# Performance work log

Hardware: AMD Instinct MI355X
Metric: run time of the kernel (lower is better)

Reference implementation:

```python
import jax, jax.numpy as jnp
import numpy as np

D_MODEL = 1024
NUM_HEADS = 16
HEAD_DIM = D_MODEL // NUM_HEADS


def setup_inputs() -> dict:
    key = jax.random.key(0)
    k_x, k_wqkv, k_bqkv, k_wo, k_bo = jax.random.split(key, 5)
    bound_qkv = 1.0 / np.sqrt(D_MODEL)
    x = jax.random.normal(k_x, (2, 2048, D_MODEL), dtype=jnp.float32)
    # torch nn.Linear init: U(-1/sqrt(fan_in), 1/sqrt(fan_in))
    W_qkv = jax.random.uniform(k_wqkv, (D_MODEL, 3 * D_MODEL), jnp.float32, -bound_qkv, bound_qkv)
    b_qkv = jax.random.uniform(k_bqkv, (3 * D_MODEL,), jnp.float32, -bound_qkv, bound_qkv)
    W_out = jax.random.uniform(k_wo, (D_MODEL, D_MODEL), jnp.float32, -bound_qkv, bound_qkv)
    b_out = jax.random.uniform(k_bo, (D_MODEL,), jnp.float32, -bound_qkv, bound_qkv)
    return {"x": x, "W_qkv": W_qkv, "b_qkv": b_qkv, "W_out": W_out, "b_out": b_out}


def reference(x, W_qkv, b_qkv, W_out, b_out):
    B, T, C = x.shape
    H, Dh = NUM_HEADS, HEAD_DIM
    qkv = x @ W_qkv + b_qkv                      # [B,T,3C]
    q, k, v = jnp.split(qkv, 3, axis=-1)
    # [B,T,C] -> [B,H,T,Dh]
    def to_heads(t):
        return t.reshape(B, T, H, Dh).transpose(0, 2, 1, 3)
    q, k, v = to_heads(q), to_heads(k), to_heads(v)
    scale = 1.0 / np.sqrt(Dh).astype(np.float32)
    scores = jnp.einsum("bhqd,bhkd->bhqk", q, k) * scale   # [B,H,T,T]
    weights = jax.nn.softmax(scores, axis=-1)
    attn = jnp.einsum("bhqk,bhkd->bhqd", weights, v)        # [B,H,T,Dh]
    attn = attn.transpose(0, 2, 1, 3).reshape(B, T, C)
    return attn @ W_out + b_out
```

## Files before the change

### kernel.cpp

```cpp
#include <hip/hip_runtime.h>

typedef __bf16 bf16x8 __attribute__((ext_vector_type(8)));
typedef float f32x4 __attribute__((ext_vector_type(4)));
typedef float f32x16 __attribute__((ext_vector_type(16)));

#define MFMA16(a, b, c) __builtin_amdgcn_mfma_f32_16x16x32_bf16(a, b, c, 0, 0, 0)
#define MFMA32(a, b, c) __builtin_amdgcn_mfma_f32_32x32x16_bf16(a, b, c, 0, 0, 0)
#define GLDS16(g, l)                                                              \
  __builtin_amdgcn_global_load_lds((const __attribute__((address_space(1))) void*)(g), \
                                   (__attribute__((address_space(3))) void*)(l), 16, 0, 0)

static __device__ __forceinline__ unsigned cvt_pk_bf16(float lo, float hi) {
  unsigned r;
  asm("v_cvt_pk_bf16_f32 %0, %1, %2" : "=v"(r) : "v"(lo), "v"(hi));
  return r;
}
static __device__ __forceinline__ void permswap(unsigned& a, unsigned& b) {
  asm("v_permlane32_swap_b32 %0, %1" : "+v"(a), "+v"(b));
}

__global__ __launch_bounds__(256) void cvt_bf16_kernel(const float* __restrict__ in,
                                                       __bf16* __restrict__ out, int n4) {
  int i = blockIdx.x * 256 + threadIdx.x;
  if (i < n4) {
    float4 v = ((const float4*)in)[i];
    union { __bf16 b[4]; uint2 u; } t;
    t.b[0] = (__bf16)v.x; t.b[1] = (__bf16)v.y;
    t.b[2] = (__bf16)v.z; t.b[3] = (__bf16)v.w;
    ((uint2*)out)[i] = t.u;
  }
}

__global__ __launch_bounds__(256) void transpose_w_kernel(const float* __restrict__ Wq,
                                                          __bf16* __restrict__ WqT,
                                                          const float* __restrict__ Wo,
                                                          __bf16* __restrict__ WoT) {
  const int Kd = 1024;
  int bx = blockIdx.x;
  const float* W; __bf16* WT; int Nd, n0;
  if (bx < 96) { W = Wq; WT = WqT; Nd = 3072; n0 = bx * 32; }
  else         { W = Wo; WT = WoT; Nd = 1024; n0 = (bx - 96) * 32; }
  __shared__ float tile[32][33];
  int k0 = blockIdx.y * 32;
  int tid = threadIdx.x;
  int kk = tid >> 3, nn = (tid & 7) * 4;
  float4 v = *(const float4*)&W[(size_t)(k0 + kk) * Nd + n0 + nn];
  tile[kk][nn] = v.x; tile[kk][nn + 1] = v.y;
  tile[kk][nn + 2] = v.z; tile[kk][nn + 3] = v.w;
  __syncthreads();
  int n2 = tid >> 3, k2 = (tid & 7) * 4;
  union { __bf16 b[4]; uint2 u; } t;
  t.b[0] = (__bf16)tile[k2][n2];
  t.b[1] = (__bf16)tile[k2 + 1][n2];
  t.b[2] = (__bf16)tile[k2 + 2][n2];
  t.b[3] = (__bf16)tile[k2 + 3][n2];
  *(uint2*)&WT[(size_t)(n0 + n2) * Kd + k0 + k2] = t.u;
}

template <bool OUT_F32, int NT>
__global__ __launch_bounds__(256) void gemm_kernel(const __bf16* __restrict__ A,
                                                   const __bf16* __restrict__ BT,
                                                   const float* __restrict__ bias,
                                                   void* __restrict__ Cout, int N,
                                                   int qn, float qs) {
  const int K = 1024;
  const int NJ = NT / 32;
  __shared__ __align__(16) __bf16 As[128 * 32];
  __shared__ __align__(16) __bf16 Bs[NT * 32];
  int tid = threadIdx.x;
  int wave = tid >> 6, lane = tid & 63;
  int quad = lane >> 4, l16 = lane & 15;
  int m0 = blockIdx.x * 128, n0 = blockIdx.y * NT;
  int wm = (wave >> 1) * 64, wn = (wave & 1) * (NT / 2);

  int srow = tid >> 2, scol = (tid & 3) * 8;
  const __bf16* aptr = A + (size_t)(m0 + srow) * K + scol;
  const __bf16* bptr = BT + (size_t)(n0 + srow) * K + scol;
  __bf16* asl = &As[(size_t)wave * 512];
  __bf16* bsl = &Bs[(size_t)wave * 512];

  f32x4 acc[4][NJ] = {};
  for (int k0 = 0; k0 < K; k0 += 32) {
    GLDS16(aptr + k0, asl);
    GLDS16(aptr + (size_t)64 * K + k0, asl + 2048);
    GLDS16(bptr + k0, bsl);
    if (NT == 128) GLDS16(bptr + (size_t)64 * K + k0, bsl + 2048);
    __syncthreads();
    bf16x8 af[4], bf[NJ];
    for (int i = 0; i < 4; i++)
      af[i] = *(bf16x8*)&As[(wm + i * 16 + l16) * 32 + quad * 8];
    for (int j = 0; j < NJ; j++)
      bf[j] = *(bf16x8*)&Bs[(wn + j * 16 + l16) * 32 + quad * 8];
    for (int i = 0; i < 4; i++)
      for (int j = 0; j < NJ; j++)
        acc[i][j] = MFMA16(af[i], bf[j], acc[i][j]);
    __syncthreads();
  }
  for (int j = 0; j < NJ; j++) {
    int col = n0 + wn + j * 16 + l16;
    float bv = bias[col];
    float sc = (col < qn) ? qs : 1.0f;
    for (int i = 0; i < 4; i++) {
      int rowb = m0 + wm + i * 16 + quad * 4;
      for (int r = 0; r < 4; r++) {
        float v = (acc[i][j][r] + bv) * sc;
        if (OUT_F32)
          ((float*)Cout)[(size_t)(rowb + r) * N + col] = v;
        else
          ((__bf16*)Cout)[(size_t)(rowb + r) * N + col] = (__bf16)v;
      }
    }
  }
}

__global__ __launch_bounds__(256) void transpose_v_kernel(const __bf16* __restrict__ qkv,
                                                          __bf16* __restrict__ Vt) {
  const int T = 2048, C3 = 3072;
  __shared__ __align__(16) __bf16 tile[64][72];
  int t0 = blockIdx.x * 64;
  int h = blockIdx.y, b = blockIdx.z;
  int tid = threadIdx.x;
  int tt = tid >> 2, c = (tid & 3) * 16;
  const __bf16* src = qkv + (size_t)(b * T + t0 + tt) * C3 + 2048 + h * 64 + c;
  *(uint4*)&tile[tt][c] = *(const uint4*)src;
  *(uint4*)&tile[tt][c + 8] = *(const uint4*)(src + 8);
  __syncthreads();
  int dd = tid >> 2, t2 = (tid & 3) * 16;
  union { __bf16 b_[16]; uint4 u[2]; } o;
  for (int i = 0; i < 16; i++) o.b_[i] = tile[t2 + i][dd];
  __bf16* dst = Vt + ((size_t)(b * 16 + h) * 64 + dd) * T + t0 + t2;
  *(uint4*)dst = o.u[0];
  *(uint4*)(dst + 8) = o.u[1];
}

__global__ __launch_bounds__(256, 2) void attn_kernel(const __bf16* __restrict__ qkv,
                                                      const __bf16* __restrict__ Vt,
                                                      __bf16* __restrict__ O) {
  const int T = 2048, C3 = 3072;
  int p = blockIdx.x * 4 + (blockIdx.y >> 4);
  int b = p >> 4, h = p & 15;
  int q0 = (blockIdx.y & 15) * 128;

  int tid = threadIdx.x, wave = tid >> 6, lane = tid & 63;
  int l32 = lane & 31, hi = lane >> 5;

  __shared__ __align__(16) __bf16 Ks[2][64 * 64];
  __shared__ __align__(16) __bf16 Vs[2][64 * 64];

  const __bf16* qp = qkv + (size_t)(b * T + q0 + wave * 32 + l32) * C3 + h * 64;
  bf16x8 qf[4];
#pragma unroll
  for (int ds = 0; ds < 4; ds++)
    qf[ds] = *(const bf16x8*)(qp + ds * 16 + hi * 8);

  const __bf16* kbase = qkv + (size_t)(b * T) * C3 + 1024 + h * 64;
  const __bf16* vbase = Vt + (size_t)(b * 16 + h) * 64 * T;

  int srow = wave * 8 + (lane >> 3);
  int scol = ((lane & 7) ^ (lane >> 3)) * 8;
  const __bf16* ksrc = kbase + (size_t)srow * C3 + scol;
  const __bf16* vsrc = vbase + (size_t)srow * T + scol;

  int off[2][4];
#pragma unroll
  for (int rb = 0; rb < 2; rb++)
#pragma unroll
    for (int c4 = 0; c4 < 4; c4++)
      off[rb][c4] = (rb * 32 + l32) * 64 + (((c4 * 2 + hi) ^ (l32 & 7)) * 8);

  f32x16 o[2] = {};
  float rs = 0.0f;

  GLDS16(ksrc, &Ks[0][wave * 512]);
  GLDS16(ksrc + (size_t)32 * C3, &Ks[0][wave * 512 + 2048]);
  GLDS16(vsrc, &Vs[0][wave * 512]);
  GLDS16(vsrc + (size_t)32 * T, &Vs[0][wave * 512 + 2048]);

#pragma unroll 2
  for (int t = 0; t < 32; t++) {
    int cur = t & 1, nxt = cur ^ 1;
    __syncthreads();
    if (t + 1 < 32) {
      const __bf16* kp = ksrc + (size_t)(t + 1) * 64 * C3;
      const __bf16* vp = vsrc + (t + 1) * 64;
      GLDS16(kp, &Ks[nxt][wave * 512]);
      GLDS16(kp + (size_t)32 * C3, &Ks[nxt][wave * 512 + 2048]);
      GLDS16(vp, &Vs[nxt][wave * 512]);
      GLDS16(vp + (size_t)32 * T, &Vs[nxt][wave * 512 + 2048]);
    }
    const __bf16* ks = &Ks[cur][0];
    const __bf16* vs = &Vs[cur][0];

    bf16x8 kf[2][4];
#pragma unroll
    for (int kb = 0; kb < 2; kb++)
#pragma unroll
      for (int ds = 0; ds < 4; ds++)
        kf[kb][ds] = *(const bf16x8*)(ks + off[kb][ds]);
    f32x16 sT[2] = {};
    __builtin_amdgcn_s_setprio(1);
#pragma unroll
    for (int kb = 0; kb < 2; kb++)
#pragma unroll
      for (int ds = 0; ds < 4; ds++)
        sT[kb] = MFMA32(kf[kb][ds], qf[ds], sT[kb]);
    __builtin_amdgcn_s_setprio(0);

    bf16x8 ap[4];
#pragma unroll
    for (int kb = 0; kb < 2; kb++) {
      float p[16];
#pragma unroll
      for (int r = 0; r < 16; r++) {
        p[r] = __builtin_amdgcn_exp2f(sT[kb][r]);
        rs += p[r];
      }
#pragma unroll
      for (int hf = 0; hf < 2; hf++) {
        unsigned w0 = cvt_pk_bf16(p[hf * 8 + 0], p[hf * 8 + 1]);
        unsigned w1 = cvt_pk_bf16(p[hf * 8 + 2], p[hf * 8 + 3]);
        unsigned w2 = cvt_pk_bf16(p[hf * 8 + 4], p[hf * 8 + 5]);
        unsigned w3 = cvt_pk_bf16(p[hf * 8 + 6], p[hf * 8 + 7]);
        permswap(w0, w2);
        permswap(w1, w3);
        union { unsigned u[4]; bf16x8 v; } pk;
        pk.u[0] = w0; pk.u[1] = w1; pk.u[2] = w2; pk.u[3] = w3;
        ap[kb * 2 + hf] = pk.v;
      }
    }

    bf16x8 vf[2][4];
#pragma unroll
    for (int db = 0; db < 2; db++)
#pragma unroll
      for (int ks2 = 0; ks2 < 4; ks2++)
        vf[db][ks2] = *(const bf16x8*)(vs + off[db][ks2]);
    __builtin_amdgcn_s_setprio(1);
#pragma unroll
    for (int db = 0; db < 2; db++)
#pragma unroll
      for (int ks2 = 0; ks2 < 4; ks2++)
        o[db] = MFMA32(ap[ks2], vf[db][ks2], o[db]);
    __builtin_amdgcn_s_setprio(0);
  }

  unsigned xu = __float_as_uint(rs), yu = __float_as_uint(rs);
  permswap(xu, yu);
  float inv = 1.0f / (__uint_as_float(xu) + __uint_as_float(yu));
  float invv[16];
#pragma unroll
  for (int r = 0; r < 16; r++)
    invv[r] = __shfl(inv, (r & 3) + 8 * (r >> 2) + 4 * hi);

  __bf16* ob = O + (size_t)(b * T + q0 + wave * 32) * 1024 + h * 64 + l32;
#pragma unroll
  for (int db = 0; db < 2; db++)
#pragma unroll
    for (int r = 0; r < 16; r++) {
      int row = (r & 3) + 8 * (r >> 2) + 4 * hi;
      ob[(size_t)row * 1024 + db * 32] = (__bf16)(o[db][r] * invv[r]);
    }
}

extern "C" void kernel_launch(void* const* d_in, const int* in_sizes, int n_in,
                              void* d_out, int out_size, void* d_ws, size_t ws_size,
                              hipStream_t stream) {
  const float* x = (const float*)d_in[0];
  const float* W_qkv = (const float*)d_in[1];
  const float* b_qkv = (const float*)d_in[2];
  const float* W_out = (const float*)d_in[3];
  const float* b_out = (const float*)d_in[4];
  float* out = (float*)d_out;

  char* ws = (char*)d_ws;
  __bf16* WqkvT = (__bf16*)(ws);
  __bf16* WoT = (__bf16*)(ws + 6291456);
  __bf16* xb = (__bf16*)(ws + 8388608);
  __bf16* qkvb = (__bf16*)(ws + 16777216);
  __bf16* Vt = (__bf16*)(ws + 41943040);
  __bf16* attnb = xb;

  const float cs = 0.125f * 1.44269504089f;

  cvt_bf16_kernel<<<4096, 256, 0, stream>>>(x, xb, 1048576);
  transpose_w_kernel<<<dim3(128, 32), 256, 0, stream>>>(W_qkv, WqkvT, W_out, WoT);
  gemm_kernel<false, 128><<<dim3(32, 24), 256, 0, stream>>>(xb, WqkvT, b_qkv, qkvb, 3072,
                                                            1024, cs);
  transpose_v_kernel<<<dim3(32, 16, 2), 256, 0, stream>>>(qkvb, Vt);
  attn_kernel<<<dim3(8, 64), 256, 0, stream>>>(qkvb, Vt, attnb);
  gemm_kernel<true, 64><<<dim3(32, 16), 256, 0, stream>>>(attnb, WoT, b_out, out, 1024,
                                                          0, 1.0f);
}
```

Before: 183.9 us.

## Triple-buffer K/V tiles and compute softmax row sums with an MFMA

Moves the attention inner loop from a double-buffered to a triple-buffered LDS pipeline. Each iteration prefetches two tiles ahead, and a partial vmcnt wait plus a raw s_barrier replaces the full __syncthreads. The softmax denominator is now accumulated by an extra MFMA against a ones vector, which removes the scalar exp sums and the final permute/shuffle reduction. V fragment loads are hoisted before the exp step. This uses more LDS, which may lower occupancy, and adds one MFMA per k-step. The row sum is now taken over the bf16-rounded probabilities.

```diff
diff --git a/kernel.cpp b/kernel.cpp
--- a/kernel.cpp
+++ b/kernel.cpp
@@ -144,8 +144,8 @@
   int tid = threadIdx.x, wave = tid >> 6, lane = tid & 63;
   int l32 = lane & 31, hi = lane >> 5;
 
-  __shared__ __align__(16) __bf16 Ks[2][64 * 64];
-  __shared__ __align__(16) __bf16 Vs[2][64 * 64];
+  __shared__ __align__(16) __bf16 Ks[3][64 * 64];
+  __shared__ __align__(16) __bf16 Vs[3][64 * 64];
 
   const __bf16* qp = qkv + (size_t)(b * T + q0 + wave * 32 + l32) * C3 + h * 64;
   bf16x8 qf[4];
@@ -169,24 +169,39 @@
       off[rb][c4] = (rb * 32 + l32) * 64 + (((c4 * 2 + hi) ^ (l32 & 7)) * 8);
 
   f32x16 o[2] = {};
-  float rs = 0.0f;
+  f32x16 lacc = {};
+  bf16x8 ones;
+#pragma unroll
+  for (int i = 0; i < 8; i++) ones[i] = (__bf16)1.0f;
 
   GLDS16(ksrc, &Ks[0][wave * 512]);
   GLDS16(ksrc + (size_t)32 * C3, &Ks[0][wave * 512 + 2048]);
   GLDS16(vsrc, &Vs[0][wave * 512]);
   GLDS16(vsrc + (size_t)32 * T, &Vs[0][wave * 512 + 2048]);
-
-#pragma unroll 2
-  for (int t = 0; t < 32; t++) {
-    int cur = t & 1, nxt = cur ^ 1;
-    __syncthreads();
-    if (t + 1 < 32) {
-      const __bf16* kp = ksrc + (size_t)(t + 1) * 64 * C3;
-      const __bf16* vp = vsrc + (t + 1) * 64;
-      GLDS16(kp, &Ks[nxt][wave * 512]);
-      GLDS16(kp + (size_t)32 * C3, &Ks[nxt][wave * 512 + 2048]);
-      GLDS16(vp, &Vs[nxt][wave * 512]);
-      GLDS16(vp + (size_t)32 * T, &Vs[nxt][wave * 512 + 2048]);
+  {
+    const __bf16* kp = ksrc + (size_t)64 * C3;
+    const __bf16* vp = vsrc + 64;
+    GLDS16(kp, &Ks[1][wave * 512]);
+    GLDS16(kp + (size_t)32 * C3, &Ks[1][wave * 512 + 2048]);
+    GLDS16(vp, &Vs[1][wave * 512]);
+    GLDS16(vp + (size_t)32 * T, &Vs[1][wave * 512 + 2048]);
+  }
+
+  int cur = 0, st = 2;
+  for (int t = 0; t < 32; ++t) {
+    if (t < 31)
+      asm volatile("s_waitcnt vmcnt(4)" ::: "memory");
+    else
+      asm volatile("s_waitcnt vmcnt(0)" ::: "memory");
+    __builtin_amdgcn_s_barrier();
+
+    if (t + 2 < 32) {
+      const __bf16* kp = ksrc + (size_t)(t + 2) * 64 * C3;
+      const __bf16* vp = vsrc + (t + 2) * 64;
+      GLDS16(kp, &Ks[st][wave * 512]);
+      GLDS16(kp + (size_t)32 * C3, &Ks[st][wave * 512 + 2048]);
+      GLDS16(vp, &Vs[st][wave * 512]);
+      GLDS16(vp + (size_t)32 * T, &Vs[st][wave * 512 + 2048]);
     }
     const __bf16* ks = &Ks[cur][0];
     const __bf16* vs = &Vs[cur][0];
@@ -206,21 +221,25 @@
         sT[kb] = MFMA32(kf[kb][ds], qf[ds], sT[kb]);
     __builtin_amdgcn_s_setprio(0);
 
+    bf16x8 vf[2][4];
+#pragma unroll
+    for (int db = 0; db < 2; db++)
+#pragma unroll
+      for (int ks2 = 0; ks2 < 4; ks2++)
+        vf[db][ks2] = *(const bf16x8*)(vs + off[db][ks2]);
+
     bf16x8 ap[4];
 #pragma unroll
     for (int kb = 0; kb < 2; kb++) {
-      float p[16];
-#pragma unroll
-      for (int r = 0; r < 16; r++) {
-        p[r] = __builtin_amdgcn_exp2f(sT[kb][r]);
-        rs += p[r];
-      }
+      float pv[16];
+#pragma unroll
+      for (int r = 0; r < 16; r++) pv[r] = __builtin_amdgcn_exp2f(sT[kb][r]);
 #pragma unroll
       for (int hf = 0; hf < 2; hf++) {
-        unsigned w0 = cvt_pk_bf16(p[hf * 8 + 0], p[hf * 8 + 1]);
-        unsigned w1 = cvt_pk_bf16(p[hf * 8 + 2], p[hf * 8 + 3]);
-        unsigned w2 = cvt_pk_bf16(p[hf * 8 + 4], p[hf * 8 + 5]);
-        unsigned w3 = cvt_pk_bf16(p[hf * 8 + 6], p[hf * 8 + 7]);
+        unsigned w0 = cvt_pk_bf16(pv[hf * 8 + 0], pv[hf * 8 + 1]);
+        unsigned w1 = cvt_pk_bf16(pv[hf * 8 + 2], pv[hf * 8 + 3]);
+        unsigned w2 = cvt_pk_bf16(pv[hf * 8 + 4], pv[hf * 8 + 5]);
+        unsigned w3 = cvt_pk_bf16(pv[hf * 8 + 6], pv[hf * 8 + 7]);
         permswap(w0, w2);
         permswap(w1, w3);
         union { unsigned u[4]; bf16x8 v; } pk;
@@ -229,37 +248,27 @@
       }
     }
 
-    bf16x8 vf[2][4];
-#pragma unroll
-    for (int db = 0; db < 2; db++)
-#pragma unroll
-      for (int ks2 = 0; ks2 < 4; ks2++)
-        vf[db][ks2] = *(const bf16x8*)(vs + off[db][ks2]);
     __builtin_amdgcn_s_setprio(1);
 #pragma unroll
-    for (int db = 0; db < 2; db++)
-#pragma unroll
-      for (int ks2 = 0; ks2 < 4; ks2++)
-        o[db] = MFMA32(ap[ks2], vf[db][ks2], o[db]);
+    for (int ks2 = 0; ks2 < 4; ks2++) {
+      o[0] = MFMA32(ap[ks2], vf[0][ks2], o[0]);
+      o[1] = MFMA32(ap[ks2], vf[1][ks2], o[1]);
+      lacc = MFMA32(ap[ks2], ones, lacc);
+    }
     __builtin_amdgcn_s_setprio(0);
-  }
-
-  unsigned xu = __float_as_uint(rs), yu = __float_as_uint(rs);
-  permswap(xu, yu);
-  float inv = 1.0f / (__uint_as_float(xu) + __uint_as_float(yu));
-  float invv[16];
-#pragma unroll
-  for (int r = 0; r < 16; r++)
-    invv[r] = __shfl(inv, (r & 3) + 8 * (r >> 2) + 4 * hi);
+
+    cur = (cur == 2) ? 0 : cur + 1;
+    st = (st == 2) ? 0 : st + 1;
+  }
 
   __bf16* ob = O + (size_t)(b * T + q0 + wave * 32) * 1024 + h * 64 + l32;
 #pragma unroll
-  for (int db = 0; db < 2; db++)
-#pragma unroll
-    for (int r = 0; r < 16; r++) {
-      int row = (r & 3) + 8 * (r >> 2) + 4 * hi;
-      ob[(size_t)row * 1024 + db * 32] = (__bf16)(o[db][r] * invv[r]);
-    }
+  for (int r = 0; r < 16; r++) {
+    float inv = 1.0f / lacc[r];
+    int row = (r & 3) + 8 * (r >> 2) + 4 * hi;
+    ob[(size_t)row * 1024] = (__bf16)(o[0][r] * inv);
+    ob[(size_t)row * 1024 + 32] = (__bf16)(o[1][r] * inv);
+  }
 }
 
 extern "C" void kernel_launch(void* const* d_in, const int* in_sizes, int n_in,
```

Result: no change. 187.0 us (+1.7%).

## Software-pipeline attention loop: overlap QK^T of next tile with softmax/PV of current

Applied to the files above, without the earlier changes.

Restructures the attention inner loop so that each iteration computes QK^T scores for tile t+1 while doing exp and PV for tile t. K is prefetched two tiles ahead and V one tile ahead, using a 4-slot LDS ring with compile-time offsets and a templated, unrolled iteration. The goal is to hide MFMA latency behind the transcendental and packing work, and to cut the LDS-wait stall. The cost is more registers for the two score buffers, and the s_setprio hints are removed, which could hurt occupancy.

```diff
diff --git a/kernel.cpp b/kernel.cpp
--- a/kernel.cpp
+++ b/kernel.cpp
@@ -133,6 +133,77 @@
   *(uint4*)(dst + 8) = o.u[1];
 }
 
+struct AttnState {
+  const char* lbase;
+  char* wdst;
+  int lb[2][4];
+};
+
+template <int KRD, int VRD, int KST, int VST, bool DO_KST>
+__device__ __forceinline__ void attn_iter(const AttnState& st, const __bf16* kg,
+                                          const __bf16* vg, const bf16x8 (&qf)[4],
+                                          const f32x16* sIN, f32x16* sOUT, f32x16& o0,
+                                          f32x16& o1, float& rs) {
+  const int T = 2048, C3 = 3072;
+  __syncthreads();
+  if constexpr (DO_KST) {
+    GLDS16(kg, st.wdst + KST);
+    GLDS16(kg + (size_t)32 * C3, st.wdst + KST + 4096);
+  }
+  GLDS16(vg, st.wdst + VST);
+  GLDS16(vg + (size_t)32 * T, st.wdst + VST + 4096);
+
+  bf16x8 kf[2][4], vf[2][4];
+#pragma unroll
+  for (int rb = 0; rb < 2; rb++)
+#pragma unroll
+    for (int ds = 0; ds < 4; ds++)
+      kf[rb][ds] = *(const bf16x8*)(st.lbase + st.lb[rb][ds] + KRD);
+#pragma unroll
+  for (int db = 0; db < 2; db++)
+#pragma unroll
+    for (int k2 = 0; k2 < 4; k2++)
+      vf[db][k2] = *(const bf16x8*)(st.lbase + st.lb[db][k2] + VRD);
+
+  f32x16 s0 = {}, s1 = {};
+#pragma unroll
+  for (int ds = 0; ds < 4; ds++) {
+    s0 = MFMA32(kf[0][ds], qf[ds], s0);
+    s1 = MFMA32(kf[1][ds], qf[ds], s1);
+  }
+  sOUT[0] = s0;
+  sOUT[1] = s1;
+
+  bf16x8 ap[4];
+#pragma unroll
+  for (int kb = 0; kb < 2; kb++) {
+    float pv[16];
+#pragma unroll
+    for (int r = 0; r < 16; r++) {
+      pv[r] = __builtin_amdgcn_exp2f(sIN[kb][r]);
+      rs += pv[r];
+    }
+#pragma unroll
+    for (int hf = 0; hf < 2; hf++) {
+      unsigned w0 = cvt_pk_bf16(pv[hf * 8 + 0], pv[hf * 8 + 1]);
+      unsigned w1 = cvt_pk_bf16(pv[hf * 8 + 2], pv[hf * 8 + 3]);
+      unsigned w2 = cvt_pk_bf16(pv[hf * 8 + 4], pv[hf * 8 + 5]);
+      unsigned w3 = cvt_pk_bf16(pv[hf * 8 + 6], pv[hf * 8 + 7]);
+      permswap(w0, w2);
+      permswap(w1, w3);
+      union { unsigned u[4]; bf16x8 v; } pk;
+      pk.u[0] = w0; pk.u[1] = w1; pk.u[2] = w2; pk.u[3] = w3;
+      ap[kb * 2 + hf] = pk.v;
+    }
+  }
+
+#pragma unroll
+  for (int k2 = 0; k2 < 4; k2++) {
+    o0 = MFMA32(ap[k2], vf[0][k2], o0);
+    o1 = MFMA32(ap[k2], vf[1][k2], o1);
+  }
+}
+
 __global__ __launch_bounds__(256, 2) void attn_kernel(const __bf16* __restrict__ qkv,
                                                       const __bf16* __restrict__ Vt,
                                                       __bf16* __restrict__ O) {
@@ -144,8 +215,7 @@
   int tid = threadIdx.x, wave = tid >> 6, lane = tid & 63;
   int l32 = lane & 31, hi = lane >> 5;
 
-  __shared__ __align__(16) __bf16 Ks[2][64 * 64];
-  __shared__ __align__(16) __bf16 Vs[2][64 * 64];
+  __shared__ __align__(16) __bf16 KV[4][64 * 64];
 
   const __bf16* qp = qkv + (size_t)(b * T + q0 + wave * 32 + l32) * C3 + h * 64;
   bf16x8 qf[4];
@@ -161,66 +231,80 @@
   const __bf16* ksrc = kbase + (size_t)srow * C3 + scol;
   const __bf16* vsrc = vbase + (size_t)srow * T + scol;
 
-  int off[2][4];
+  AttnState st;
+  st.lbase = (const char*)&KV[0][0];
+  st.wdst = (char*)&KV[0][0] + wave * 1024;
 #pragma unroll
   for (int rb = 0; rb < 2; rb++)
 #pragma unroll
     for (int c4 = 0; c4 < 4; c4++)
-      off[rb][c4] = (rb * 32 + l32) * 64 + (((c4 * 2 + hi) ^ (l32 & 7)) * 8);
-
-  f32x16 o[2] = {};
+      st.lb[rb][c4] =
+          ((rb * 32 + l32) * 64 + (((c4 * 2 + hi) ^ (l32 & 7)) * 8)) * 2;
+
+  f32x16 o0 = {}, o1 = {};
+  f32x16 sA[2], sB[2];
   float rs = 0.0f;
 
-  GLDS16(ksrc, &Ks[0][wave * 512]);
-  GLDS16(ksrc + (size_t)32 * C3, &Ks[0][wave * 512 + 2048]);
-  GLDS16(vsrc, &Vs[0][wave * 512]);
-  GLDS16(vsrc + (size_t)32 * T, &Vs[0][wave * 512 + 2048]);
-
-#pragma unroll 2
-  for (int t = 0; t < 32; t++) {
-    int cur = t & 1, nxt = cur ^ 1;
+  GLDS16(ksrc, st.wdst + 0);
+  GLDS16(ksrc + (size_t)32 * C3, st.wdst + 4096);
+  GLDS16(vsrc, st.wdst + 8192);
+  GLDS16(vsrc + (size_t)32 * T, st.wdst + 8192 + 4096);
+  GLDS16(ksrc + (size_t)64 * C3, st.wdst + 16384);
+  GLDS16(ksrc + (size_t)96 * C3, st.wdst + 16384 + 4096);
+  __syncthreads();
+
+  {
+    bf16x8 kf[2][4];
+#pragma unroll
+    for (int rb = 0; rb < 2; rb++)
+#pragma unroll
+      for (int ds = 0; ds < 4; ds++)
+        kf[rb][ds] = *(const bf16x8*)(st.lbase + st.lb[rb][ds] + 0);
+    f32x16 s0 = {}, s1 = {};
+#pragma unroll
+    for (int ds = 0; ds < 4; ds++) {
+      s0 = MFMA32(kf[0][ds], qf[ds], s0);
+      s1 = MFMA32(kf[1][ds], qf[ds], s1);
+    }
+    sA[0] = s0;
+    sA[1] = s1;
+  }
+
+  const size_t kstep = (size_t)64 * C3;
+  const __bf16* kg = ksrc + 2 * kstep;
+  const __bf16* vg = vsrc + 64;
+
+  for (int tp = 0; tp < 15; ++tp) {
+    attn_iter<16384, 8192, 0, 24576, true>(st, kg, vg, qf, sA, sB, o0, o1, rs);
+    kg += kstep; vg += 64;
+    attn_iter<0, 24576, 16384, 8192, true>(st, kg, vg, qf, sB, sA, o0, o1, rs);
+    kg += kstep; vg += 64;
+  }
+  attn_iter<16384, 8192, 0, 24576, false>(st, kg, vg, qf, sA, sB, o0, o1, rs);
+
+  {
     __syncthreads();
-    if (t + 1 < 32) {
-      const __bf16* kp = ksrc + (size_t)(t + 1) * 64 * C3;
-      const __bf16* vp = vsrc + (t + 1) * 64;
-      GLDS16(kp, &Ks[nxt][wave * 512]);
-      GLDS16(kp + (size_t)32 * C3, &Ks[nxt][wave * 512 + 2048]);
-      GLDS16(vp, &Vs[nxt][wave * 512]);
-      GLDS16(vp + (size_t)32 * T, &Vs[nxt][wave * 512 + 2048]);
-    }
-    const __bf16* ks = &Ks[cur][0];
-    const __bf16* vs = &Vs[cur][0];
-
-    bf16x8 kf[2][4];
-#pragma unroll
-    for (int kb = 0; kb < 2; kb++)
-#pragma unroll
-      for (int ds = 0; ds < 4; ds++)
-        kf[kb][ds] = *(const bf16x8*)(ks + off[kb][ds]);
-    f32x16 sT[2] = {};
-    __builtin_amdgcn_s_setprio(1);
-#pragma unroll
-    for (int kb = 0; kb < 2; kb++)
-#pragma unroll
-      for (int ds = 0; ds < 4; ds++)
-        sT[kb] = MFMA32(kf[kb][ds], qf[ds], sT[kb]);
-    __builtin_amdgcn_s_setprio(0);
-
+    bf16x8 vf[2][4];
+#pragma unroll
+    for (int db = 0; db < 2; db++)
+#pragma unroll
+      for (int k2 = 0; k2 < 4; k2++)
+        vf[db][k2] = *(const bf16x8*)(st.lbase + st.lb[db][k2] + 24576);
     bf16x8 ap[4];
 #pragma unroll
     for (int kb = 0; kb < 2; kb++) {
-      float p[16];
+      float pv[16];
 #pragma unroll
       for (int r = 0; r < 16; r++) {
-        p[r] = __builtin_amdgcn_exp2f(sT[kb][r]);
-        rs += p[r];
+        pv[r] = __builtin_amdgcn_exp2f(sB[kb][r]);
+        rs += pv[r];
       }
 #pragma unroll
       for (int hf = 0; hf < 2; hf++) {
-        unsigned w0 = cvt_pk_bf16(p[hf * 8 + 0], p[hf * 8 + 1]);
-        unsigned w1 = cvt_pk_bf16(p[hf * 8 + 2], p[hf * 8 + 3]);
-        unsigned w2 = cvt_pk_bf16(p[hf * 8 + 4], p[hf * 8 + 5]);
-        unsigned w3 = cvt_pk_bf16(p[hf * 8 + 6], p[hf * 8 + 7]);
+        unsigned w0 = cvt_pk_bf16(pv[hf * 8 + 0], pv[hf * 8 + 1]);
+        unsigned w1 = cvt_pk_bf16(pv[hf * 8 + 2], pv[hf * 8 + 3]);
+        unsigned w2 = cvt_pk_bf16(pv[hf * 8 + 4], pv[hf * 8 + 5]);
+        unsigned w3 = cvt_pk_bf16(pv[hf * 8 + 6], pv[hf * 8 + 7]);
         permswap(w0, w2);
         permswap(w1, w3);
         union { unsigned u[4]; bf16x8 v; } pk;
@@ -228,20 +312,11 @@
         ap[kb * 2 + hf] = pk.v;
       }
     }
-
-    bf16x8 vf[2][4];
-#pragma unroll
-    for (int db = 0; db < 2; db++)
-#pragma unroll
-      for (int ks2 = 0; ks2 < 4; ks2++)
-        vf[db][ks2] = *(const bf16x8*)(vs + off[db][ks2]);
-    __builtin_amdgcn_s_setprio(1);
-#pragma unroll
-    for (int db = 0; db < 2; db++)
-#pragma unroll
-      for (int ks2 = 0; ks2 < 4; ks2++)
-        o[db] = MFMA32(ap[ks2], vf[db][ks2], o[db]);
-    __builtin_amdgcn_s_setprio(0);
+#pragma unroll
+    for (int k2 = 0; k2 < 4; k2++) {
+      o0 = MFMA32(ap[k2], vf[0][k2], o0);
+      o1 = MFMA32(ap[k2], vf[1][k2], o1);
+    }
   }
 
   unsigned xu = __float_as_uint(rs), yu = __float_as_uint(rs);
@@ -254,12 +329,11 @@
 
   __bf16* ob = O + (size_t)(b * T + q0 + wave * 32) * 1024 + h * 64 + l32;
 #pragma unroll
-  for (int db = 0; db < 2; db++)
-#pragma unroll
-    for (int r = 0; r < 16; r++) {
-      int row = (r & 3) + 8 * (r >> 2) + 4 * hi;
-      ob[(size_t)row * 1024 + db * 32] = (__bf16)(o[db][r] * invv[r]);
-    }
+  for (int r = 0; r < 16; r++) {
+    int row = (r & 3) + 8 * (r >> 2) + 4 * hi;
+    ob[(size_t)row * 1024] = (__bf16)(o0[r] * invv[r]);
+    ob[(size_t)row * 1024 + 32] = (__bf16)(o1[r] * invv[r]);
+  }
 }
 
 extern "C" void kernel_launch(void* const* d_in, const int* in_sizes, int n_in,
```

New measurement: 179.1 us. -2.6%, faster.
